# Optimization experiments

Hardware: AMD Instinct MI355X
Metric: run time of the kernel (lower is better)

## Reference

```python
import jax, jax.numpy as jnp
import numpy as np
from jax import lax


def _conv(x, w):
    # 3x3 conv, stride 1, SAME padding, NCHW/OIHW layout, no bias
    return lax.conv_general_dilated(
        x, w, window_strides=(1, 1), padding='SAME',
        dimension_numbers=('NCHW', 'OIHW', 'NCHW'))


def _interleave2x2(tl, tr, bl, br):
    # each [B,H,W] -> [B,2H,2W] with tl at (0::2,0::2), tr at (0::2,1::2), etc.
    top = jnp.stack([tl, tr], axis=-1)          # [B,H,W,2]
    bot = jnp.stack([bl, br], axis=-1)          # [B,H,W,2]
    x = jnp.stack([top, bot], axis=2)           # [B,H,2,W,2]
    B, H, _, W, _ = x.shape
    return x.reshape(B, 2 * H, 2 * W)


def setup_inputs() -> dict:
    key = jax.random.key(0)
    ks = jax.random.split(key, 8)
    B, H, W = 16, 512, 512
    width = 12
    s = 0.1  # weight scale, approximates xavier for tiny fan-ins
    return {
        'mosaic': jax.random.normal(ks[0], (B, 4, H, W), jnp.float32),
        'fw0': jax.random.normal(ks[1], (width, 4, 3, 3), jnp.float32) * s,
        'fw1': jax.random.normal(ks[2], (width, width, 3, 3), jnp.float32) * s,
        'fw2': jax.random.normal(ks[3], (width, width, 3, 3), jnp.float32) * s,
        'ww0': jax.random.normal(ks[4], (width, 4, 3, 3), jnp.float32) * s,
        'ww1': jax.random.normal(ks[5], (width, width, 3, 3), jnp.float32) * s,
        'ww2': jax.random.normal(ks[6], (width, width, 3, 3), jnp.float32) * s,
        'cw0': jax.random.normal(ks[7], (6, 2, 3, 3), jnp.float32) * s,
    }


def reference(mosaic, fw0, fw1, fw2, ww0, ww1, ww2, cw0):
    width = fw0.shape[0]  # 12
    half = width // 2

    f = jax.nn.relu(_conv(mosaic, fw0))
    f = jax.nn.relu(_conv(f, fw1))
    interps = jax.nn.relu(_conv(f, fw2))

    w = jax.nn.relu(_conv(mosaic, ww0))
    w = jax.nn.relu(_conv(w, ww1))
    w = jax.nn.relu(_conv(w, ww2))
    weights = jax.nn.softmax(w, axis=1)

    mul = interps * weights                              # [B,12,H,W]
    # green_rb[:,0] = sum of first half, green_rb[:,1] = sum of second half
    green_rb = jnp.stack(
        [mul[:, :half].sum(axis=1), mul[:, half:].sum(axis=1)], axis=1)  # [B,2,H,W]

    # green_add channels: [mosaic0, g1, mosaic3, mosaic0, g0, mosaic3]
    green_add = jnp.stack([
        mosaic[:, 0], green_rb[:, 1], mosaic[:, 3],
        mosaic[:, 0], green_rb[:, 0], mosaic[:, 3]], axis=1)  # [B,6,H,W]

    # chroma: (rb - green_rb) -> single conv 2->6 (chroma_depth=1, no relu)
    rb = jnp.stack([mosaic[:, 1], mosaic[:, 2]], axis=1)  # [B,2,H,W]
    chroma_diff = _conv(rb - green_rb, cw0)               # [B,6,H,W]
    chroma_pred = chroma_diff + green_add

    # pixel-shuffle assembly of full-res RGB [B,3,2H,2W]
    r = _interleave2x2(chroma_pred[:, 0], mosaic[:, 1], chroma_pred[:, 1], chroma_pred[:, 2])
    g = _interleave2x2(mosaic[:, 0], green_rb[:, 0], green_rb[:, 1], mosaic[:, 3])
    b = _interleave2x2(chroma_pred[:, 3], chroma_pred[:, 4], mosaic[:, 2], chroma_pred[:, 5])
    return jnp.stack([r, g, b], axis=1)
```

## Files before the change

kernel.cpp:

```cpp
#include <hip/hip_runtime.h>
#include <cstdint>

#define HH 512
#define WW 512
#define TX 60

typedef __attribute__((ext_vector_type(8)))  short    short8;
typedef __attribute__((ext_vector_type(16))) float    f32x16;
typedef __attribute__((ext_vector_type(2)))  unsigned u32x2;
typedef long long lng;

union FragU { uint4 u; short8 s; };
union U4L   { uint4 u; lng l[2]; };
union B8U   { u32x2 u2[2]; short8 s; };
union BL    { unsigned w[2]; lng l; };

#define L1F_O  0
#define L1W_O  9216
#define L1RST  768
#define MOS_O  18432
#define MOSR   528
#define L2F_O  18432
#define L2W_O  25872
#define L2RST  744
#define RELAY_O 0
#define SMEMB  33312

__device__ __forceinline__ unsigned cvtpk(float a, float b) {
  unsigned r;
  asm("v_cvt_pk_bf16_f32 %0, %1, %2" : "=v"(r) : "v"(a), "v"(b));
  return r;
}
__device__ __forceinline__ unsigned rpk8(float a, float b, float c, float d, bool im) {
  int r = __builtin_amdgcn_cvt_pk_fp8_f32(fmaxf(a, 0.f), fmaxf(b, 0.f), 0, false);
  r = __builtin_amdgcn_cvt_pk_fp8_f32(fmaxf(c, 0.f), fmaxf(d, 0.f), r, true);
  return im ? (unsigned)r : 0u;
}
__device__ __forceinline__ unsigned short f2bf(float f) {
  union { float f; unsigned u; } v; v.f = f;
  unsigned r = v.u + 0x7fffu + ((v.u >> 16) & 1u);
  return (unsigned short)(r >> 16);
}
__device__ __forceinline__ float bf2f(unsigned short b) {
  union { unsigned u; float f; } v; v.u = ((unsigned)b) << 16;
  return v.f;
}
__device__ __forceinline__ float lo16(unsigned u) {
  union { unsigned v; float f; } x; x.v = u << 16; return x.f;
}
__device__ __forceinline__ float hi16(unsigned u) {
  union { unsigned v; float f; } x; x.v = u & 0xffff0000u; return x.f;
}
__device__ __forceinline__ lng rd8(const char* p) {
  BL t;
  t.w[0] = *(const unsigned*)p;
  t.w[1] = *(const unsigned*)(p + 4);
  return t.l;
}

__global__ void wt_kernel(const float* __restrict__ fw0, const float* __restrict__ fw1,
                          const float* __restrict__ fw2, const float* __restrict__ ww0,
                          const float* __restrict__ ww1, const float* __restrict__ ww2,
                          uint4* __restrict__ wsf) {
  int t = blockIdx.x * 256 + threadIdx.x;
  if (t >= 31 * 64) return;
  int f = t >> 6, lane = t & 63;
  int h = (lane >> 5) & 1, m = lane & 31;
  uint4 o = make_uint4(0, 0, 0, 0);
  if (f < 3) {
    unsigned short v[8];
#pragma unroll
    for (int e = 0; e < 8; ++e) {
      int sq = 2 * h + (e >> 2);
      int c4 = e & 3;
      float w = 0.f;
      if (sq < 3 && m < 24) {
        w = (m < 12) ? fw0[(m * 4 + c4) * 9 + f * 3 + sq]
                     : ww0[((m - 12) * 4 + c4) * 9 + f * 3 + sq];
      }
      v[e] = f2bf(w);
    }
    o.x = (unsigned)v[0] | ((unsigned)v[1] << 16);
    o.y = (unsigned)v[2] | ((unsigned)v[3] << 16);
    o.z = (unsigned)v[4] | ((unsigned)v[5] << 16);
    o.w = (unsigned)v[6] | ((unsigned)v[7] << 16);
  } else {
    const int PR[7][2][2] = {
      {{0, 1}, {2, 3}}, {{4, 5}, {6, 7}}, {{9, 10}, {11, 12}},
      {{13, 14}, {15, 16}}, {{18, 19}, {20, 21}}, {{22, 23}, {24, 25}},
      {{8, 17}, {26, -1}}};
    int fi = f - 3, layer = fi / 14, path = (fi % 14) / 7, j = fi % 7;
    const float* src = layer ? (path ? ww2 : fw2) : (path ? ww1 : fw1);
    float wv[8];
#pragma unroll
    for (int p = 0; p < 8; ++p) {
      int q = PR[j][h][p >> 2];
      int c = p & 3;
      float w = 0.f;
      if (q >= 0 && m < 12) {
        int kap = 4 * q + c;
        int tap = kap / 12, ci = kap % 12;
        w = src[(m * 12 + ci) * 9 + tap];
      }
      wv[p] = w;
    }
    int x = __builtin_amdgcn_cvt_pk_fp8_f32(wv[0], wv[1], 0, false);
    x = __builtin_amdgcn_cvt_pk_fp8_f32(wv[2], wv[3], x, true);
    int y = __builtin_amdgcn_cvt_pk_fp8_f32(wv[4], wv[5], 0, false);
    y = __builtin_amdgcn_cvt_pk_fp8_f32(wv[6], wv[7], y, true);
    o.x = (unsigned)x; o.y = (unsigned)y;
  }
  wsf[t] = o;
}

template<int RST, int WIN>
__device__ __forceinline__ void conv12f8(const lng* aF, const lng* aW,
                                         const char* Ph, const char* Pa, const char* Pb,
                                         int imm, f32x16& cF, f32x16& cW) {
  const int IM[6] = {0, 16, RST, RST + 16, 2 * RST, 2 * RST + 16};
#pragma unroll
  for (int j = 0; j < 6; ++j) {
    lng bF = rd8(Ph + imm + IM[j]);
    lng bW = rd8(Ph + imm + IM[j] + WIN);
    cF = __builtin_amdgcn_mfma_f32_32x32x16_fp8_fp8(aF[j], bF, cF, 0, 0, 0);
    cW = __builtin_amdgcn_mfma_f32_32x32x16_fp8_fp8(aW[j], bW, cW, 0, 0, 0);
  }
  {
    BL bF, bW;
    bF.w[0] = *(const unsigned*)(Pa + imm + 32);
    bF.w[1] = *(const unsigned*)(Pb + imm + 32);
    bW.w[0] = *(const unsigned*)(Pa + imm + 32 + WIN);
    bW.w[1] = *(const unsigned*)(Pb + imm + 32 + WIN);
    cF = __builtin_amdgcn_mfma_f32_32x32x16_fp8_fp8(aF[6], bF.l, cF, 0, 0, 0);
    cW = __builtin_amdgcn_mfma_f32_32x32x16_fp8_fp8(aW[6], bW.l, cW, 0, 0, 0);
  }
}

template<int WOUT>
__device__ __forceinline__ void store12f8(char* pO, int imm, const f32x16& cF,
                                          const f32x16& cW, bool im, int h) {
  *(unsigned*)(pO + imm) = rpk8(cF[0], cF[1], cF[2], cF[3], im);
  *(unsigned*)(pO + imm + WOUT) = rpk8(cW[0], cW[1], cW[2], cW[3], im);
  if (h == 0) {
    *(unsigned*)(pO + imm + 8) = rpk8(cF[4], cF[5], cF[6], cF[7], im);
    *(unsigned*)(pO + imm + WOUT + 8) = rpk8(cW[4], cW[5], cW[6], cW[7], im);
  }
}

__global__ __launch_bounds__(256, 4)
void green_kernel(const float* __restrict__ mosaic, const uint4* __restrict__ wsf,
                  unsigned short* __restrict__ green) {
  __shared__ __align__(16) char s[SMEMB];
  const int tid = threadIdx.x;
  const int lane = tid & 63;
  const int wv = __builtin_amdgcn_readfirstlane(tid >> 6);
  const int h = (lane >> 5) & 1, ln = lane & 31;
  const int ln8 = ln * 8, ln12 = ln * 12;
  const int bid = blockIdx.x;
  const int bx = bid % 9;
  const int t9 = bid / 9;
  const int by = t9 & 63, b = t9 >> 6;
  const int X0 = bx * TX, Y0 = by * 8;

  {
    const float* mb = mosaic + (size_t)b * 4 * HH * WW;
    for (int p = tid; p < 14 * 66; p += 256) {
      int row = p / 66, col = p - row * 66;
      int gy = Y0 + row - 3, gx = X0 + col - 3;
      float c0 = 0.f, c1 = 0.f, c2 = 0.f, c3 = 0.f;
      if ((unsigned)gy < HH && (unsigned)gx < WW) {
        const float* mp = mb + (size_t)gy * WW + gx;
        c0 = mp[0]; c1 = mp[HH * WW]; c2 = mp[2 * HH * WW]; c3 = mp[3 * HH * WW];
      }
      u32x2 w = { cvtpk(c0, c1), cvtpk(c2, c3) };
      *(u32x2*)(s + MOS_O + row * MOSR + col * 8) = w;
    }
  }
  __syncthreads();

  {
    FragU a3[3];
#pragma unroll
    for (int q = 0; q < 3; ++q) a3[q].u = wsf[q * 64 + lane];
    const char* pLo = s + MOS_O + 3 * wv * MOSR + ln8 + 16 * h;
    const char* pHi = s + MOS_O + 3 * wv * MOSR + ln8 + 8;
    char* base = s + 3 * wv * L1RST + ln12;
    char* pA = base + L1F_O + 4 * h;
    char* pB = h ? base + L1W_O : base + L1F_O + 8;
    char* pC = base + L1W_O + (h ? 8 : 4);
    bool ck[2];
    ck[0] = (unsigned)(X0 + 0  + ln - 2) < WW;
    ck[1] = (unsigned)(X0 + 32 + ln - 2) < WW;
#pragma unroll
    for (int r = 0; r < 3; ++r) {
      const int ly = 3 * wv + r;
      const bool rowok = (unsigned)(Y0 + ly - 2) < HH;
#pragma unroll
      for (int g = 0; g < 2; ++g) {
        const int cb = g * 32;
        f32x16 c = {};
#pragma unroll
        for (int ky = 0; ky < 3; ++ky) {
          B8U bu;
          bu.u2[0] = *(const u32x2*)(pLo + (r + ky) * MOSR + cb * 8);
          bu.u2[1] = *(const u32x2*)(pHi + (r + ky) * MOSR + cb * 8);
          c = __builtin_amdgcn_mfma_f32_32x32x16_bf16(a3[ky].s, bu.s, c, 0, 0, 0);
        }
        const bool im = rowok && ck[g];
        *(unsigned*)(pA + r * L1RST + cb * 12) = rpk8(c[0], c[1], c[2], c[3], im);
        *(unsigned*)(pB + r * L1RST + cb * 12) = rpk8(c[4], c[5], c[6], c[7], im);
        *(unsigned*)(pC + r * L1RST + cb * 12) = rpk8(c[8], c[9], c[10], c[11], im);
      }
    }
  }
  __syncthreads();

  {
    lng aF[7], aW[7];
#pragma unroll
    for (int j = 0; j < 7; ++j) {
      U4L u; u.u = wsf[(3 + j) * 64 + lane];  aF[j] = u.l[0];
      U4L v; v.u = wsf[(10 + j) * 64 + lane]; aW[j] = v.l[0];
    }
    const char* base = s + L1F_O + wv * L1RST + ln12;
    const char* Ph = base + 8 * h;
    const char* Pa = base + (h ? 2 * L1RST : 0);
    const char* Pb = base + (h ? 2 * L1RST : L1RST);
    char* bO0 = s + L2F_O + wv * L2RST + ln12 + 4 * h;
    bool ck[2];
    ck[0] = (unsigned)(X0 + 0  + ln - 1) < WW;
    ck[1] = (unsigned)(X0 + 30 + ln - 1) < WW;
#pragma unroll
    for (int i = 0; i < 3; ++i) {
      const int ly = wv + 4 * i;
      if (ly < 10) {
        const bool rowok = (unsigned)(Y0 + ly - 1) < HH;
#pragma unroll
        for (int g = 0; g < 2; ++g) {
          const int cb = g * 30;
          f32x16 cF = {}, cW = {};
          conv12f8<L1RST, 9216>(aF, aW, Ph, Pa, Pb, i * 4 * L1RST + cb * 12, cF, cW);
          store12f8<7440>(bO0, i * 4 * L2RST + cb * 12, cF, cW, rowok && ck[g], h);
        }
      }
    }
  }
  __syncthreads();

  {
    lng aF[7], aW[7];
#pragma unroll
    for (int j = 0; j < 7; ++j) {
      U4L u; u.u = wsf[(17 + j) * 64 + lane]; aF[j] = u.l[0];
      U4L v; v.u = wsf[(24 + j) * 64 + lane]; aW[j] = v.l[0];
    }
    const char* base = s + L2F_O + 2 * wv * L2RST + ln12;
    const char* Ph = base + 8 * h;
    const char* Pa = base + (h ? 2 * L2RST : 0);
    const char* Pb = base + (h ? 2 * L2RST : L2RST);
    char* slot = s + RELAY_O + (wv * 32 + ln) * 48;
#pragma unroll
    for (int r = 0; r < 2; ++r) {
#pragma unroll
      for (int g = 0; g < 2; ++g) {
        const int cb = g * 28;
        f32x16 cF = {}, cW = {};
        conv12f8<L2RST, 7440>(aF, aW, Ph, Pa, Pb, r * L2RST + cb * 12, cF, cW);
        const int cidx = (r * 2 + g) & 1;
        if (cidx == 0) {
          if (h) {
            uint4 pay;
            pay.x = cvtpk(fmaxf(cF[0], 0.f), fmaxf(cF[1], 0.f));
            pay.y = cvtpk(fmaxf(cF[2], 0.f), fmaxf(cF[3], 0.f));
            pay.z = cvtpk(fmaxf(cW[0], 0.f), fmaxf(cW[1], 0.f));
            pay.w = cvtpk(fmaxf(cW[2], 0.f), fmaxf(cW[3], 0.f));
            *(uint4*)slot = pay;
          }
        } else {
          if (!h) {
            uint4 pa, pb;
            pa.x = cvtpk(fmaxf(cF[0], 0.f), fmaxf(cF[1], 0.f));
            pa.y = cvtpk(fmaxf(cF[2], 0.f), fmaxf(cF[3], 0.f));
            pa.z = cvtpk(fmaxf(cF[4], 0.f), fmaxf(cF[5], 0.f));
            pa.w = cvtpk(fmaxf(cF[6], 0.f), fmaxf(cF[7], 0.f));
            pb.x = cvtpk(fmaxf(cW[0], 0.f), fmaxf(cW[1], 0.f));
            pb.y = cvtpk(fmaxf(cW[2], 0.f), fmaxf(cW[3], 0.f));
            pb.z = cvtpk(fmaxf(cW[4], 0.f), fmaxf(cW[5], 0.f));
            pb.w = cvtpk(fmaxf(cW[6], 0.f), fmaxf(cW[7], 0.f));
            *(uint4*)slot = pa;
            *(uint4*)(slot + 16) = pb;
          }
        }
        asm volatile("s_waitcnt lgkmcnt(0)" ::: "memory");
        if (h == cidx) {
          float F[12], Wv[12];
          if (cidx == 0) {
            const uint4 pay = *(const uint4*)slot;
#pragma unroll
            for (int c2 = 0; c2 < 4; ++c2) {
              F[c2]      = fmaxf(cF[c2], 0.f);
              F[8 + c2]  = fmaxf(cF[4 + c2], 0.f);
              Wv[c2]     = fmaxf(cW[c2], 0.f);
              Wv[8 + c2] = fmaxf(cW[4 + c2], 0.f);
            }
            F[4] = lo16(pay.x);  F[5] = hi16(pay.x);
            F[6] = lo16(pay.y);  F[7] = hi16(pay.y);
            Wv[4] = lo16(pay.z); Wv[5] = hi16(pay.z);
            Wv[6] = lo16(pay.w); Wv[7] = hi16(pay.w);
          } else {
            const uint4 pa = *(const uint4*)slot;
            const uint4 pb = *(const uint4*)(slot + 16);
#pragma unroll
            for (int c2 = 0; c2 < 4; ++c2) {
              F[4 + c2]  = fmaxf(cF[c2], 0.f);
              Wv[4 + c2] = fmaxf(cW[c2], 0.f);
            }
            F[0] = lo16(pa.x);   F[1] = hi16(pa.x);
            F[2] = lo16(pa.y);   F[3] = hi16(pa.y);
            F[8] = lo16(pa.z);   F[9] = hi16(pa.z);
            F[10] = lo16(pa.w);  F[11] = hi16(pa.w);
            Wv[0] = lo16(pb.x);  Wv[1] = hi16(pb.x);
            Wv[2] = lo16(pb.y);  Wv[3] = hi16(pb.y);
            Wv[8] = lo16(pb.z);  Wv[9] = hi16(pb.z);
            Wv[10] = lo16(pb.w); Wv[11] = hi16(pb.w);
          }
          float m = 0.f;
#pragma unroll
          for (int c2 = 0; c2 < 12; ++c2) m = fmaxf(m, Wv[c2]);
          float sum = 0.f, s0 = 0.f, s1 = 0.f;
#pragma unroll
          for (int c2 = 0; c2 < 12; ++c2) {
            const float e = __expf(Wv[c2] - m);
            sum += e;
            if (c2 < 6) s0 = fmaf(F[c2], e, s0);
            else        s1 = fmaf(F[c2], e, s1);
          }
          const float inv = 1.f / sum;
          const unsigned pg = cvtpk(s0 * inv, s1 * inv);
          const int gy = Y0 + 2 * wv + r;
          const int gx = X0 + cb + ln;
          if ((unsigned)gx < WW) {
            green[((b * 2 + 0) * HH + gy) * WW + gx] = (unsigned short)pg;
            green[((b * 2 + 1) * HH + gy) * WW + gx] = (unsigned short)(pg >> 16);
          }
        }
      }
    }
  }
}

__global__ __launch_bounds__(256)
void assemble_kernel(const float* __restrict__ mosaic, const unsigned short* __restrict__ green,
                     const float* __restrict__ cw0, float* __restrict__ out) {
  const int t = blockIdx.x * 256 + threadIdx.x;
  const int x = t & (WW - 1);
  const int y = (t >> 9) & (HH - 1);
  const int b = t >> 18;

  const int p = y * WW + x;
  const float* __restrict__ mb = mosaic + (size_t)b * 4 * HH * WW;
  const unsigned short* __restrict__ gb = green + (size_t)b * 2 * HH * WW;

  const float m0 = mb[p];
  const float m1 = mb[HH * WW + p];
  const float m2 = mb[2 * HH * WW + p];
  const float m3 = mb[3 * HH * WW + p];
  const float g0 = bf2f(gb[p]);
  const float g1 = bf2f(gb[HH * WW + p]);

  float cd[6] = {0.f, 0.f, 0.f, 0.f, 0.f, 0.f};
#pragma unroll
  for (int ky = 0; ky < 3; ++ky) {
#pragma unroll
    for (int kx = 0; kx < 3; ++kx) {
      const int yy = y + ky - 1, xx = x + kx - 1;
      float c0 = 0.f, c1 = 0.f;
      if ((unsigned)yy < HH && (unsigned)xx < WW) {
        const int q = yy * WW + xx;
        c0 = mb[HH * WW + q]     - bf2f(gb[q]);
        c1 = mb[2 * HH * WW + q] - bf2f(gb[HH * WW + q]);
      }
      const int k = ky * 3 + kx;
#pragma unroll
      for (int o = 0; o < 6; ++o) {
        cd[o] = fmaf(c0, cw0[(o * 2 + 0) * 9 + k], cd[o]);
        cd[o] = fmaf(c1, cw0[(o * 2 + 1) * 9 + k], cd[o]);
      }
    }
  }
  const float cp0 = cd[0] + m0;
  const float cp1 = cd[1] + g1;
  const float cp2 = cd[2] + m3;
  const float cp3 = cd[3] + m0;
  const float cp4 = cd[4] + g0;
  const float cp5 = cd[5] + m3;

  const int W2 = 2 * WW;
  const size_t plane = (size_t)(2 * HH) * W2;
  size_t base = ((size_t)(b * 3) * (2 * HH) + 2 * y) * W2 + 2 * x;
  *(float2*)(out + base)              = make_float2(cp0, m1);
  *(float2*)(out + base + W2)         = make_float2(cp1, cp2);
  *(float2*)(out + base + plane)      = make_float2(m0, g0);
  *(float2*)(out + base + plane + W2) = make_float2(g1, m3);
  *(float2*)(out + base + 2 * plane)      = make_float2(cp3, cp4);
  *(float2*)(out + base + 2 * plane + W2) = make_float2(m2, cp5);
}

extern "C" void kernel_launch(void* const* d_in, const int* in_sizes, int n_in,
                              void* d_out, int out_size, void* d_ws, size_t ws_size,
                              hipStream_t stream) {
  const float* mosaic = (const float*)d_in[0];
  const float* fw0 = (const float*)d_in[1];
  const float* fw1 = (const float*)d_in[2];
  const float* fw2 = (const float*)d_in[3];
  const float* ww0 = (const float*)d_in[4];
  const float* ww1 = (const float*)d_in[5];
  const float* ww2 = (const float*)d_in[6];
  const float* cw0 = (const float*)d_in[7];

  uint4* wsf = (uint4*)((char*)d_ws + 32768);
  unsigned short* green = (unsigned short*)((char*)d_ws + 67584);
  float* out = (float*)d_out;

  wt_kernel<<<8, 256, 0, stream>>>(fw0, fw1, fw2, ww0, ww1, ww2, wsf);
  green_kernel<<<16 * 64 * 9, 256, 0, stream>>>(mosaic, wsf, green);
  assemble_kernel<<<(16 * HH * WW) / 256, 256, 0, stream>>>(mosaic, green, cw0, out);
}
```

Before: 216.7 us.

## Halve green kernel tile width to one MFMA column group, double occupancy

The green kernel tile shrinks from 60 to 28 output columns, so each wave runs a single 32-column MFMA group per row instead of two. Shared memory drops to about 17 KB and launch bounds rise to 8 blocks per CU, with 19 column blocks per row strip. The halo overhead per output grows: 34 loaded columns for 28 outputs versus 66 for 60, so more redundant conv work and mosaic reads are done. Separately, the last weight-path layer's weights are prescaled by log2(e) so the softmax can use exp2f instead of __expf.

```diff
diff --git a/kernel.cpp b/kernel.cpp
--- a/kernel.cpp
+++ b/kernel.cpp
@@ -3,7 +3,7 @@
 
 #define HH 512
 #define WW 512
-#define TX 60
+#define TX 28
 
 typedef __attribute__((ext_vector_type(8)))  short    short8;
 typedef __attribute__((ext_vector_type(16))) float    f32x16;
@@ -16,15 +16,15 @@
 union BL    { unsigned w[2]; lng l; };
 
 #define L1F_O  0
-#define L1W_O  9216
-#define L1RST  768
-#define MOS_O  18432
-#define MOSR   528
-#define L2F_O  18432
-#define L2W_O  25872
-#define L2RST  744
+#define L1W_O  4608
+#define L1RST  384
+#define MOS_O  9216
+#define MOSR   272
+#define L2F_O  9216
+#define L2W_O  13296
+#define L2RST  408
 #define RELAY_O 0
-#define SMEMB  33312
+#define SMEMB  17376
 
 __device__ __forceinline__ unsigned cvtpk(float a, float b) {
   unsigned r;
@@ -91,6 +91,7 @@
       {{8, 17}, {26, -1}}};
     int fi = f - 3, layer = fi / 14, path = (fi % 14) / 7, j = fi % 7;
     const float* src = layer ? (path ? ww2 : fw2) : (path ? ww1 : fw1);
+    const float scale = (layer == 1 && path == 1) ? 1.44269504f : 1.0f;
     float wv[8];
 #pragma unroll
     for (int p = 0; p < 8; ++p) {
@@ -100,7 +101,7 @@
       if (q >= 0 && m < 12) {
         int kap = 4 * q + c;
         int tap = kap / 12, ci = kap % 12;
-        w = src[(m * 12 + ci) * 9 + tap];
+        w = src[(m * 12 + ci) * 9 + tap] * scale;
       }
       wv[p] = w;
     }
@@ -147,7 +148,7 @@
   }
 }
 
-__global__ __launch_bounds__(256, 4)
+__global__ __launch_bounds__(256, 8)
 void green_kernel(const float* __restrict__ mosaic, const uint4* __restrict__ wsf,
                   unsigned short* __restrict__ green) {
   __shared__ __align__(16) char s[SMEMB];
@@ -157,15 +158,15 @@
   const int h = (lane >> 5) & 1, ln = lane & 31;
   const int ln8 = ln * 8, ln12 = ln * 12;
   const int bid = blockIdx.x;
-  const int bx = bid % 9;
-  const int t9 = bid / 9;
-  const int by = t9 & 63, b = t9 >> 6;
+  const int bx = bid % 19;
+  const int t19 = bid / 19;
+  const int by = t19 & 63, b = t19 >> 6;
   const int X0 = bx * TX, Y0 = by * 8;
 
   {
     const float* mb = mosaic + (size_t)b * 4 * HH * WW;
-    for (int p = tid; p < 14 * 66; p += 256) {
-      int row = p / 66, col = p - row * 66;
+    for (int p = tid; p < 14 * 34; p += 256) {
+      int row = p / 34, col = p - row * 34;
       int gy = Y0 + row - 3, gx = X0 + col - 3;
       float c0 = 0.f, c1 = 0.f, c2 = 0.f, c3 = 0.f;
       if ((unsigned)gy < HH && (unsigned)gx < WW) {
@@ -188,29 +189,23 @@
     char* pA = base + L1F_O + 4 * h;
     char* pB = h ? base + L1W_O : base + L1F_O + 8;
     char* pC = base + L1W_O + (h ? 8 : 4);
-    bool ck[2];
-    ck[0] = (unsigned)(X0 + 0  + ln - 2) < WW;
-    ck[1] = (unsigned)(X0 + 32 + ln - 2) < WW;
+    const bool ckx = (unsigned)(X0 + ln - 2) < WW;
 #pragma unroll
     for (int r = 0; r < 3; ++r) {
       const int ly = 3 * wv + r;
       const bool rowok = (unsigned)(Y0 + ly - 2) < HH;
-#pragma unroll
-      for (int g = 0; g < 2; ++g) {
-        const int cb = g * 32;
-        f32x16 c = {};
-#pragma unroll
-        for (int ky = 0; ky < 3; ++ky) {
-          B8U bu;
-          bu.u2[0] = *(const u32x2*)(pLo + (r + ky) * MOSR + cb * 8);
-          bu.u2[1] = *(const u32x2*)(pHi + (r + ky) * MOSR + cb * 8);
-          c = __builtin_amdgcn_mfma_f32_32x32x16_bf16(a3[ky].s, bu.s, c, 0, 0, 0);
-        }
-        const bool im = rowok && ck[g];
-        *(unsigned*)(pA + r * L1RST + cb * 12) = rpk8(c[0], c[1], c[2], c[3], im);
-        *(unsigned*)(pB + r * L1RST + cb * 12) = rpk8(c[4], c[5], c[6], c[7], im);
-        *(unsigned*)(pC + r * L1RST + cb * 12) = rpk8(c[8], c[9], c[10], c[11], im);
-      }
+      f32x16 c = {};
+#pragma unroll
+      for (int ky = 0; ky < 3; ++ky) {
+        B8U bu;
+        bu.u2[0] = *(const u32x2*)(pLo + (r + ky) * MOSR);
+        bu.u2[1] = *(const u32x2*)(pHi + (r + ky) * MOSR);
+        c = __builtin_amdgcn_mfma_f32_32x32x16_bf16(a3[ky].s, bu.s, c, 0, 0, 0);
+      }
+      const bool im = rowok && ckx;
+      *(unsigned*)(pA + r * L1RST) = rpk8(c[0], c[1], c[2], c[3], im);
+      *(unsigned*)(pB + r * L1RST) = rpk8(c[4], c[5], c[6], c[7], im);
+      *(unsigned*)(pC + r * L1RST) = rpk8(c[8], c[9], c[10], c[11], im);
     }
   }
   __syncthreads();
@@ -227,21 +222,15 @@
     const char* Pa = base + (h ? 2 * L1RST : 0);
     const char* Pb = base + (h ? 2 * L1RST : L1RST);
     char* bO0 = s + L2F_O + wv * L2RST + ln12 + 4 * h;
-    bool ck[2];
-    ck[0] = (unsigned)(X0 + 0  + ln - 1) < WW;
-    ck[1] = (unsigned)(X0 + 30 + ln - 1) < WW;
+    const bool ckx = (unsigned)(X0 + ln - 1) < WW;
 #pragma unroll
     for (int i = 0; i < 3; ++i) {
       const int ly = wv + 4 * i;
       if (ly < 10) {
         const bool rowok = (unsigned)(Y0 + ly - 1) < HH;
-#pragma unroll
-        for (int g = 0; g < 2; ++g) {
-          const int cb = g * 30;
-          f32x16 cF = {}, cW = {};
-          conv12f8<L1RST, 9216>(aF, aW, Ph, Pa, Pb, i * 4 * L1RST + cb * 12, cF, cW);
-          store12f8<7440>(bO0, i * 4 * L2RST + cb * 12, cF, cW, rowok && ck[g], h);
-        }
+        f32x16 cF = {}, cW = {};
+        conv12f8<L1RST, 4608>(aF, aW, Ph, Pa, Pb, i * 4 * L1RST, cF, cW);
+        store12f8<4080>(bO0, i * 4 * L2RST, cF, cW, rowok && ckx, h);
       }
     }
   }
@@ -261,88 +250,84 @@
     char* slot = s + RELAY_O + (wv * 32 + ln) * 48;
 #pragma unroll
     for (int r = 0; r < 2; ++r) {
-#pragma unroll
-      for (int g = 0; g < 2; ++g) {
-        const int cb = g * 28;
-        f32x16 cF = {}, cW = {};
-        conv12f8<L2RST, 7440>(aF, aW, Ph, Pa, Pb, r * L2RST + cb * 12, cF, cW);
-        const int cidx = (r * 2 + g) & 1;
+      f32x16 cF = {}, cW = {};
+      conv12f8<L2RST, 4080>(aF, aW, Ph, Pa, Pb, r * L2RST, cF, cW);
+      const int cidx = r;
+      if (cidx == 0) {
+        if (h) {
+          uint4 pay;
+          pay.x = cvtpk(fmaxf(cF[0], 0.f), fmaxf(cF[1], 0.f));
+          pay.y = cvtpk(fmaxf(cF[2], 0.f), fmaxf(cF[3], 0.f));
+          pay.z = cvtpk(fmaxf(cW[0], 0.f), fmaxf(cW[1], 0.f));
+          pay.w = cvtpk(fmaxf(cW[2], 0.f), fmaxf(cW[3], 0.f));
+          *(uint4*)slot = pay;
+        }
+      } else {
+        if (!h) {
+          uint4 pa, pb;
+          pa.x = cvtpk(fmaxf(cF[0], 0.f), fmaxf(cF[1], 0.f));
+          pa.y = cvtpk(fmaxf(cF[2], 0.f), fmaxf(cF[3], 0.f));
+          pa.z = cvtpk(fmaxf(cF[4], 0.f), fmaxf(cF[5], 0.f));
+          pa.w = cvtpk(fmaxf(cF[6], 0.f), fmaxf(cF[7], 0.f));
+          pb.x = cvtpk(fmaxf(cW[0], 0.f), fmaxf(cW[1], 0.f));
+          pb.y = cvtpk(fmaxf(cW[2], 0.f), fmaxf(cW[3], 0.f));
+          pb.z = cvtpk(fmaxf(cW[4], 0.f), fmaxf(cW[5], 0.f));
+          pb.w = cvtpk(fmaxf(cW[6], 0.f), fmaxf(cW[7], 0.f));
+          *(uint4*)slot = pa;
+          *(uint4*)(slot + 16) = pb;
+        }
+      }
+      asm volatile("s_waitcnt lgkmcnt(0)" ::: "memory");
+      if (h == cidx) {
+        float F[12], Wv[12];
         if (cidx == 0) {
-          if (h) {
-            uint4 pay;
-            pay.x = cvtpk(fmaxf(cF[0], 0.f), fmaxf(cF[1], 0.f));
-            pay.y = cvtpk(fmaxf(cF[2], 0.f), fmaxf(cF[3], 0.f));
-            pay.z = cvtpk(fmaxf(cW[0], 0.f), fmaxf(cW[1], 0.f));
-            pay.w = cvtpk(fmaxf(cW[2], 0.f), fmaxf(cW[3], 0.f));
-            *(uint4*)slot = pay;
+          const uint4 pay = *(const uint4*)slot;
+#pragma unroll
+          for (int c2 = 0; c2 < 4; ++c2) {
+            F[c2]      = fmaxf(cF[c2], 0.f);
+            F[8 + c2]  = fmaxf(cF[4 + c2], 0.f);
+            Wv[c2]     = fmaxf(cW[c2], 0.f);
+            Wv[8 + c2] = fmaxf(cW[4 + c2], 0.f);
           }
+          F[4] = lo16(pay.x);  F[5] = hi16(pay.x);
+          F[6] = lo16(pay.y);  F[7] = hi16(pay.y);
+          Wv[4] = lo16(pay.z); Wv[5] = hi16(pay.z);
+          Wv[6] = lo16(pay.w); Wv[7] = hi16(pay.w);
         } else {
-          if (!h) {
-            uint4 pa, pb;
-            pa.x = cvtpk(fmaxf(cF[0], 0.f), fmaxf(cF[1], 0.f));
-            pa.y = cvtpk(fmaxf(cF[2], 0.f), fmaxf(cF[3], 0.f));
-            pa.z = cvtpk(fmaxf(cF[4], 0.f), fmaxf(cF[5], 0.f));
-            pa.w = cvtpk(fmaxf(cF[6], 0.f), fmaxf(cF[7], 0.f));
-            pb.x = cvtpk(fmaxf(cW[0], 0.f), fmaxf(cW[1], 0.f));
-            pb.y = cvtpk(fmaxf(cW[2], 0.f), fmaxf(cW[3], 0.f));
-            pb.z = cvtpk(fmaxf(cW[4], 0.f), fmaxf(cW[5], 0.f));
-            pb.w = cvtpk(fmaxf(cW[6], 0.f), fmaxf(cW[7], 0.f));
-            *(uint4*)slot = pa;
-            *(uint4*)(slot + 16) = pb;
+          const uint4 pa = *(const uint4*)slot;
+          const uint4 pb = *(const uint4*)(slot + 16);
+#pragma unroll
+          for (int c2 = 0; c2 < 4; ++c2) {
+            F[4 + c2]  = fmaxf(cF[c2], 0.f);
+            Wv[4 + c2] = fmaxf(cW[c2], 0.f);
           }
+          F[0] = lo16(pa.x);   F[1] = hi16(pa.x);
+          F[2] = lo16(pa.y);   F[3] = hi16(pa.y);
+          F[8] = lo16(pa.z);   F[9] = hi16(pa.z);
+          F[10] = lo16(pa.w);  F[11] = hi16(pa.w);
+          Wv[0] = lo16(pb.x);  Wv[1] = hi16(pb.x);
+          Wv[2] = lo16(pb.y);  Wv[3] = hi16(pb.y);
+          Wv[8] = lo16(pb.z);  Wv[9] = hi16(pb.z);
+          Wv[10] = lo16(pb.w); Wv[11] = hi16(pb.w);
         }
-        asm volatile("s_waitcnt lgkmcnt(0)" ::: "memory");
-        if (h == cidx) {
-          float F[12], Wv[12];
-          if (cidx == 0) {
-            const uint4 pay = *(const uint4*)slot;
-#pragma unroll
-            for (int c2 = 0; c2 < 4; ++c2) {
-              F[c2]      = fmaxf(cF[c2], 0.f);
-              F[8 + c2]  = fmaxf(cF[4 + c2], 0.f);
-              Wv[c2]     = fmaxf(cW[c2], 0.f);
-              Wv[8 + c2] = fmaxf(cW[4 + c2], 0.f);
-            }
-            F[4] = lo16(pay.x);  F[5] = hi16(pay.x);
-            F[6] = lo16(pay.y);  F[7] = hi16(pay.y);
-            Wv[4] = lo16(pay.z); Wv[5] = hi16(pay.z);
-            Wv[6] = lo16(pay.w); Wv[7] = hi16(pay.w);
-          } else {
-            const uint4 pa = *(const uint4*)slot;
-            const uint4 pb = *(const uint4*)(slot + 16);
-#pragma unroll
-            for (int c2 = 0; c2 < 4; ++c2) {
-              F[4 + c2]  = fmaxf(cF[c2], 0.f);
-              Wv[4 + c2] = fmaxf(cW[c2], 0.f);
-            }
-            F[0] = lo16(pa.x);   F[1] = hi16(pa.x);
-            F[2] = lo16(pa.y);   F[3] = hi16(pa.y);
-            F[8] = lo16(pa.z);   F[9] = hi16(pa.z);
-            F[10] = lo16(pa.w);  F[11] = hi16(pa.w);
-            Wv[0] = lo16(pb.x);  Wv[1] = hi16(pb.x);
-            Wv[2] = lo16(pb.y);  Wv[3] = hi16(pb.y);
-            Wv[8] = lo16(pb.z);  Wv[9] = hi16(pb.z);
-            Wv[10] = lo16(pb.w); Wv[11] = hi16(pb.w);
-          }
-          float m = 0.f;
-#pragma unroll
-          for (int c2 = 0; c2 < 12; ++c2) m = fmaxf(m, Wv[c2]);
-          float sum = 0.f, s0 = 0.f, s1 = 0.f;
-#pragma unroll
-          for (int c2 = 0; c2 < 12; ++c2) {
-            const float e = __expf(Wv[c2] - m);
-            sum += e;
-            if (c2 < 6) s0 = fmaf(F[c2], e, s0);
-            else        s1 = fmaf(F[c2], e, s1);
-          }
-          const float inv = 1.f / sum;
-          const unsigned pg = cvtpk(s0 * inv, s1 * inv);
-          const int gy = Y0 + 2 * wv + r;
-          const int gx = X0 + cb + ln;
-          if ((unsigned)gx < WW) {
-            green[((b * 2 + 0) * HH + gy) * WW + gx] = (unsigned short)pg;
-            green[((b * 2 + 1) * HH + gy) * WW + gx] = (unsigned short)(pg >> 16);
-          }
+        float m = 0.f;
+#pragma unroll
+        for (int c2 = 0; c2 < 12; ++c2) m = fmaxf(m, Wv[c2]);
+        float sum = 0.f, s0 = 0.f, s1 = 0.f;
+#pragma unroll
+        for (int c2 = 0; c2 < 12; ++c2) {
+          const float e = exp2f(Wv[c2] - m);
+          sum += e;
+          if (c2 < 6) s0 = fmaf(F[c2], e, s0);
+          else        s1 = fmaf(F[c2], e, s1);
+        }
+        const float inv = 1.f / sum;
+        const unsigned pg = cvtpk(s0 * inv, s1 * inv);
+        const int gy = Y0 + 2 * wv + r;
+        const int gx = X0 + ln;
+        if (ln < TX && (unsigned)gx < WW) {
+          green[((b * 2 + 0) * HH + gy) * WW + gx] = (unsigned short)pg;
+          green[((b * 2 + 1) * HH + gy) * WW + gx] = (unsigned short)(pg >> 16);
         }
       }
     }
@@ -423,6 +408,6 @@
   float* out = (float*)d_out;
 
   wt_kernel<<<8, 256, 0, stream>>>(fw0, fw1, fw2, ww0, ww1, ww2, wsf);
-  green_kernel<<<16 * 64 * 9, 256, 0, stream>>>(mosaic, wsf, green);
+  green_kernel<<<16 * 64 * 19, 256, 0, stream>>>(mosaic, wsf, green);
   assemble_kernel<<<(16 * HH * WW) / 256, 256, 0, stream>>>(mosaic, green, cw0, out);
 }
```

After: 300.4 us. +38.6%, slower.
